# Kernel optimization log

Measured on AMD Instinct MI355X. Metric: run time of the kernel, lower is better.

The kernel has to match this reference:

```python
import jax, jax.numpy as jnp
import numpy as np

TAU = 2.0
V_TH = 1.0
ATAN_ALPHA = 2.0
LN_EPS = 1e-5

# Surrogate-gradient spike: forward = Heaviside(v - v_th), backward = ATan surrogate
@jax.custom_vjp
def atan_spike(x):
    return (x >= 0.0).astype(x.dtype)

def _atan_spike_fwd(x):
    return atan_spike(x), x

def _atan_spike_bwd(x, g):
    grad = ATAN_ALPHA / (2.0 * (1.0 + (jnp.pi / 2.0 * ATAN_ALPHA * x) ** 2))
    return (g * grad,)

atan_spike.defvjp(_atan_spike_fwd, _atan_spike_bwd)

def layernorm(x, g, b):
    m = jnp.mean(x, axis=-1, keepdims=True)
    v = jnp.mean((x - m) ** 2, axis=-1, keepdims=True)
    return (x - m) * jax.lax.rsqrt(v + LN_EPS) * g + b

def lif_multistep(x_btd):
    """spikingjelly LIFNode: decay_input=True, v_reset=0.0 (hard reset), detach_reset=True.
    x_btd: [B, T, D]; scan over T with membrane state [B, D]; returns spikes [B, T, D]."""
    x_tbd = jnp.swapaxes(x_btd, 0, 1)  # [T, B, D]
    def step(v, xt):
        h = v + (xt - v) / TAU                      # charge (decay_input, v_reset=0)
        s = atan_spike(h - V_TH)                    # fire
        v_new = h * (1.0 - jax.lax.stop_gradient(s))  # hard reset to 0, detached spike
        return v_new, s
    _, spikes = jax.lax.scan(step, jnp.zeros_like(x_tbd[0]), x_tbd)
    return jnp.swapaxes(spikes, 0, 1)  # [B, T, D]

def setup_inputs() -> dict:
    key = jax.random.key(0)
    ks = jax.random.split(key, 3)
    B, T, D, H = 256, 256, 128, 256
    x = jax.random.normal(ks[0], (B, T, D), dtype=jnp.float32)
    W1 = jax.random.normal(ks[1], (H, D), dtype=jnp.float32) * (1.0 / np.sqrt(D))
    b1 = jnp.zeros((H,), jnp.float32)
    g1 = jnp.ones((H,), jnp.float32)
    be1 = jnp.zeros((H,), jnp.float32)
    W2 = jax.random.normal(ks[2], (D, H), dtype=jnp.float32) * (1.0 / np.sqrt(H))
    b2 = jnp.zeros((D,), jnp.float32)
    g2 = jnp.ones((D,), jnp.float32)
    be2 = jnp.zeros((D,), jnp.float32)
    return {"x": x, "W1": W1, "b1": b1, "g1": g1, "be1": be1,
            "W2": W2, "b2": b2, "g2": g2, "be2": be2}

def reference(x, W1, b1, g1, be1, W2, b2, g2, be2):
    residual = x
    h = jnp.einsum("btd,hd->bth", x, W1) + b1
    h = layernorm(h, g1, be1)
    h = lif_multistep(h)            # dropout is identity at eval
    o = jnp.einsum("bth,dh->btd", h, W2) + b2
    o = layernorm(o, g2, be2)
    o = lif_multistep(o)
    return residual + o
```

## Files before the change

kernel.cpp:

```cpp
#include <hip/hip_runtime.h>
#include <hip/hip_bf16.h>
#include <stdint.h>

#define B_ 256
#define T_ 256
#define D_ 128
#define H_ 256
#define LN_EPS 1e-5

__global__ __launch_bounds__(256, 2) void k1_gemm_ln(
    const float* __restrict__ x, const float* __restrict__ W1,
    const float* __restrict__ b1, const float* __restrict__ g1, const float* __restrict__ be1,
    double* __restrict__ h1, int row0)
{
  __shared__ double As[16][64];
  __shared__ double Bs[16][256];
  const int tid = threadIdx.x;
  const int tx = tid & 31, ty = tid >> 5;
  const int orow = blockIdx.x * 64;
  const int grow = row0 + orow;

  double acc[8][8];
  #pragma unroll
  for (int i = 0; i < 8; ++i)
    #pragma unroll
    for (int j = 0; j < 8; ++j) acc[i][j] = 0.0;

  for (int kt = 0; kt < 128; kt += 16) {
    __syncthreads();
    {
      const int row = tid >> 2, ko = (tid & 3) * 4;
      const float4 f = *(const float4*)(x + (size_t)(grow + row) * 128 + kt + ko);
      As[ko+0][row] = (double)f.x; As[ko+1][row] = (double)f.y;
      As[ko+2][row] = (double)f.z; As[ko+3][row] = (double)f.w;
    }
    {
      const float* src = W1 + (size_t)tid * 128 + kt;
      #pragma unroll
      for (int j = 0; j < 4; ++j) {
        const float4 f = *(const float4*)(src + j*4);
        Bs[j*4+0][tid] = (double)f.x; Bs[j*4+1][tid] = (double)f.y;
        Bs[j*4+2][tid] = (double)f.z; Bs[j*4+3][tid] = (double)f.w;
      }
    }
    __syncthreads();
    #pragma unroll 2
    for (int k = 0; k < 16; ++k) {
      double a[8], b[8];
      #pragma unroll
      for (int j = 0; j < 4; ++j) {
        const double2 t2 = *(const double2*)&As[k][ty*8 + j*2];
        a[j*2] = t2.x; a[j*2+1] = t2.y;
      }
      #pragma unroll
      for (int c = 0; c < 4; ++c) {
        const double2 t2 = *(const double2*)&Bs[k][c*64 + tx*2];
        b[c*2] = t2.x; b[c*2+1] = t2.y;
      }
      #pragma unroll
      for (int i = 0; i < 8; ++i)
        #pragma unroll
        for (int j = 0; j < 8; ++j)
          acc[i][j] = fma(a[i], b[j], acc[i][j]);
    }
  }

  double gg[8], ee[8];
  #pragma unroll
  for (int j = 0; j < 8; ++j) {
    const int col = (j >> 1)*64 + tx*2 + (j & 1);
    const double bb = (double)b1[col];
    gg[j] = (double)g1[col]; ee[j] = (double)be1[col];
    #pragma unroll
    for (int i = 0; i < 8; ++i) acc[i][j] += bb;
  }
  #pragma unroll
  for (int i = 0; i < 8; ++i) {
    double s = 0.0, q = 0.0;
    #pragma unroll
    for (int j = 0; j < 8; ++j) { s += acc[i][j]; q += acc[i][j]*acc[i][j]; }
    #pragma unroll
    for (int m = 16; m >= 1; m >>= 1) { s += __shfl_xor(s, m, 64); q += __shfl_xor(q, m, 64); }
    const double mean = s * (1.0/256.0);
    const double var  = q * (1.0/256.0) - mean*mean;
    const double rstd = 1.0 / sqrt(var + LN_EPS);
    const int r = orow + ty*8 + i;
    #pragma unroll
    for (int c = 0; c < 4; ++c) {
      double2 o;
      o.x = (acc[i][c*2+0] - mean) * rstd * gg[c*2+0] + ee[c*2+0];
      o.y = (acc[i][c*2+1] - mean) * rstd * gg[c*2+1] + ee[c*2+1];
      *(double2*)&h1[(size_t)r*256 + c*64 + tx*2] = o;
    }
  }
}

__global__ __launch_bounds__(256) void k2_lif(
    const double* __restrict__ h1, uint8_t* __restrict__ s1)
{
  const int ci = blockIdx.x * 256 + threadIdx.x;
  const int b = ci >> 8, h = ci & 255;
  const double* p = h1 + (size_t)b * (T_*H_) + h;
  uint8_t* qp = s1 + (size_t)b * (T_*H_) + h;
  double v = 0.0;
  #pragma unroll 8
  for (int t = 0; t < T_; ++t) {
    const double xv = p[(size_t)t * H_];
    const double hm = v + (xv - v) * 0.5;
    const bool s = (hm >= 1.0);
    v = s ? 0.0 : hm;
    qp[(size_t)t * H_] = s ? (uint8_t)1 : (uint8_t)0;
  }
}

__global__ __launch_bounds__(256, 2) void k3_gemm_ln(
    const uint8_t* __restrict__ s1, const float* __restrict__ W2,
    const float* __restrict__ b2, const float* __restrict__ g2, const float* __restrict__ be2,
    double* __restrict__ h2)
{
  __shared__ double As[32][64];
  __shared__ double Bs[32][128];
  const int tid = threadIdx.x;
  const int tx = tid & 31, ty = tid >> 5;
  const int orow = blockIdx.x * 64;

  double acc[8][4];
  #pragma unroll
  for (int i = 0; i < 8; ++i)
    #pragma unroll
    for (int j = 0; j < 4; ++j) acc[i][j] = 0.0;

  for (int kt = 0; kt < 256; kt += 32) {
    __syncthreads();
    {
      const int row = tid >> 2, ko = (tid & 3) * 8;
      const uint2 u = *(const uint2*)(s1 + (size_t)(orow + row) * 256 + kt + ko);
      #pragma unroll
      for (int j = 0; j < 4; ++j) As[ko+j][row]   = (double)((u.x >> (8*j)) & 0xffu);
      #pragma unroll
      for (int j = 0; j < 4; ++j) As[ko+4+j][row] = (double)((u.y >> (8*j)) & 0xffu);
    }
    {
      const int col = tid >> 1, k0 = (tid & 1) * 16;
      const float* src = W2 + (size_t)col * 256 + kt + k0;
      #pragma unroll
      for (int j = 0; j < 4; ++j) {
        const float4 f = *(const float4*)(src + j*4);
        Bs[k0+j*4+0][col] = (double)f.x; Bs[k0+j*4+1][col] = (double)f.y;
        Bs[k0+j*4+2][col] = (double)f.z; Bs[k0+j*4+3][col] = (double)f.w;
      }
    }
    __syncthreads();
    #pragma unroll 2
    for (int k = 0; k < 32; ++k) {
      double a[8], b[4];
      #pragma unroll
      for (int j = 0; j < 4; ++j) {
        const double2 t2 = *(const double2*)&As[k][ty*8 + j*2];
        a[j*2] = t2.x; a[j*2+1] = t2.y;
      }
      #pragma unroll
      for (int c = 0; c < 2; ++c) {
        const double2 t2 = *(const double2*)&Bs[k][c*64 + tx*2];
        b[c*2] = t2.x; b[c*2+1] = t2.y;
      }
      #pragma unroll
      for (int i = 0; i < 8; ++i)
        #pragma unroll
        for (int j = 0; j < 4; ++j)
          acc[i][j] = fma(a[i], b[j], acc[i][j]);
    }
  }

  double gg[4], ee[4];
  #pragma unroll
  for (int j = 0; j < 4; ++j) {
    const int col = (j >> 1)*64 + tx*2 + (j & 1);
    const double bb = (double)b2[col];
    gg[j] = (double)g2[col]; ee[j] = (double)be2[col];
    #pragma unroll
    for (int i = 0; i < 8; ++i) acc[i][j] += bb;
  }
  #pragma unroll
  for (int i = 0; i < 8; ++i) {
    double s = 0.0, q = 0.0;
    #pragma unroll
    for (int j = 0; j < 4; ++j) { s += acc[i][j]; q += acc[i][j]*acc[i][j]; }
    #pragma unroll
    for (int m = 16; m >= 1; m >>= 1) { s += __shfl_xor(s, m, 64); q += __shfl_xor(q, m, 64); }
    const double mean = s * (1.0/128.0);
    const double var  = q * (1.0/128.0) - mean*mean;
    const double rstd = 1.0 / sqrt(var + LN_EPS);
    const int r = orow + ty*8 + i;
    #pragma unroll
    for (int c = 0; c < 2; ++c) {
      double2 o;
      o.x = (acc[i][c*2+0] - mean)*rstd*gg[c*2+0] + ee[c*2+0];
      o.y = (acc[i][c*2+1] - mean)*rstd*gg[c*2+1] + ee[c*2+1];
      *(double2*)&h2[(size_t)r*128 + c*64 + tx*2] = o;
    }
  }
}

__global__ __launch_bounds__(64) void k4_lif_res(
    const double* __restrict__ h2, const float* __restrict__ x,
    float* __restrict__ out, int row0)
{
  const int ci = blockIdx.x * 64 + threadIdx.x;
  const int b = ci >> 7, d = ci & 127;
  const double* p = h2 + (size_t)b * (T_*D_) + d;
  const size_t gbase = ((size_t)row0 + (size_t)b * T_) * D_ + d;
  double v = 0.0;
  #pragma unroll 8
  for (int t = 0; t < T_; ++t) {
    const double hv = p[(size_t)t * D_];
    const double hm = v + (hv - v) * 0.5;
    const bool s = (hm >= 1.0);
    v = s ? 0.0 : hm;
    out[gbase + (size_t)t * D_] = x[gbase + (size_t)t * D_] + (s ? 1.0f : 0.0f);
  }
}

extern "C" void kernel_launch(void* const* d_in, const int* in_sizes, int n_in,
                              void* d_out, int out_size, void* d_ws, size_t ws_size,
                              hipStream_t stream)
{
  const float* x   = (const float*)d_in[0];
  const float* W1  = (const float*)d_in[1];
  const float* b1  = (const float*)d_in[2];
  const float* g1  = (const float*)d_in[3];
  const float* be1 = (const float*)d_in[4];
  const float* W2  = (const float*)d_in[5];
  const float* b2  = (const float*)d_in[6];
  const float* g2  = (const float*)d_in[7];
  const float* be2 = (const float*)d_in[8];
  float* out = (float*)d_out;

  const size_t per_b = (size_t)T_*H_*sizeof(double) + (size_t)T_*H_ + (size_t)T_*D_*sizeof(double);
  int Bc = B_;
  while (Bc > 1 && (size_t)Bc * per_b > ws_size) Bc >>= 1;

  double*  h1 = (double*)d_ws;
  uint8_t* s1 = (uint8_t*)d_ws + (size_t)Bc*T_*H_*sizeof(double);
  double*  h2 = (double*)((uint8_t*)d_ws + (size_t)Bc*T_*H_*sizeof(double) + (size_t)Bc*T_*H_);

  const int nchunk = B_ / Bc;
  for (int c = 0; c < nchunk; ++c) {
    const int row0 = c * Bc * T_;
    k1_gemm_ln<<<dim3(Bc*4), dim3(256), 0, stream>>>(x, W1, b1, g1, be1, h1, row0);
    k2_lif   <<<dim3(Bc),   dim3(256), 0, stream>>>(h1, s1);
    k3_gemm_ln<<<dim3(Bc*4), dim3(256), 0, stream>>>(s1, W2, b2, g2, be2, h2);
    k4_lif_res<<<dim3(Bc*2), dim3(64),  0, stream>>>(h2, x, out, row0);
  }
}
```

Baseline: 333.3 us.

## Use FP64 MFMA 16x16x4 for both GEMM+LayerNorm kernels with runtime layout probe

Replaces the scalar FP64 FMA register-tiled GEMMs in k1 and k3 with __builtin_amdgcn_mfma_f64_16x16x4f64 matrix instructions, one 16-row strip per wave. A runtime probe discovers the accumulator row mapping and falls back to a scalar path if the layout is unexpected. Shared tiles are padded to reduce bank conflicts, and the k3 K-tile shrinks to 16. It aims to cut the dominant FP64 GEMM compute cost, at the price of probe overhead, scalar strided output stores, and heavier register use.

```diff
diff --git a/kernel.cpp b/kernel.cpp
--- a/kernel.cpp
+++ b/kernel.cpp
@@ -8,89 +8,153 @@
 #define H_ 256
 #define LN_EPS 1e-5
 
+typedef double f64x4 __attribute__((ext_vector_type(4)));
+
+__device__ __forceinline__ bool probe_f64_mfma_layout(int l16, int lg, int* rowp)
+{
+  const f64x4 zz = {0.0, 0.0, 0.0, 0.0};
+  const double pa_r = (lg == 0) ? (double)l16 : 0.0;
+  const double pb_1 = (lg == 0) ? 1.0 : 0.0;
+  const f64x4 prow = __builtin_amdgcn_mfma_f64_16x16x4f64(pa_r, pb_1, zz, 0, 0, 0);
+  const double pa_1 = (lg == 0) ? 1.0 : 0.0;
+  const double pb_c = (lg == 0) ? (double)l16 : 0.0;
+  const f64x4 pcol = __builtin_amdgcn_mfma_f64_16x16x4f64(pa_1, pb_c, zz, 0, 0, 0);
+  bool ok = true;
+  int rm = 0, rp = 0;
+  #pragma unroll
+  for (int r = 0; r < 4; ++r) {
+    const int ri = (int)prow[r];
+    const int ci = (int)pcol[r];
+    rowp[r] = ri;
+    ok = ok && ((double)ri == prow[r]) && (ri >= 0) && (ri < 16);
+    ok = ok && ((double)ci == pcol[r]) && (ci == l16);
+    rm |= 1 << ri;
+    rp |= ri << (4 * r);
+  }
+  ok = ok && (__popc(rm) == 4);
+  #pragma unroll
+  for (int m = 1; m <= 8; m <<= 1)
+    ok = ok && (__shfl_xor(rp, m, 64) == rp);
+  int rmw = rm;
+  rmw |= __shfl_xor(rmw, 16, 64);
+  rmw |= __shfl_xor(rmw, 32, 64);
+  ok = ok && (rmw == 0xFFFF);
+  return __all((int)ok) != 0;
+}
+
 __global__ __launch_bounds__(256, 2) void k1_gemm_ln(
     const float* __restrict__ x, const float* __restrict__ W1,
     const float* __restrict__ b1, const float* __restrict__ g1, const float* __restrict__ be1,
     double* __restrict__ h1, int row0)
 {
-  __shared__ double As[16][64];
-  __shared__ double Bs[16][256];
-  const int tid = threadIdx.x;
-  const int tx = tid & 31, ty = tid >> 5;
+  __shared__ double As[16 * 66];
+  __shared__ double Bs[16 * 258];
+  const int tid  = threadIdx.x;
+  const int lane = tid & 63, wave = tid >> 6;
+  const int l16  = lane & 15, lg = lane >> 4;
   const int orow = blockIdx.x * 64;
   const int grow = row0 + orow;
-
-  double acc[8][8];
-  #pragma unroll
-  for (int i = 0; i < 8; ++i)
-    #pragma unroll
-    for (int j = 0; j < 8; ++j) acc[i][j] = 0.0;
-
-  for (int kt = 0; kt < 128; kt += 16) {
+  const int wrow = wave * 16;
+
+  int rowp[4];
+  const bool ok = probe_f64_mfma_layout(l16, lg, rowp);
+
+  auto stage = [&](int kt) {
     __syncthreads();
     {
       const int row = tid >> 2, ko = (tid & 3) * 4;
       const float4 f = *(const float4*)(x + (size_t)(grow + row) * 128 + kt + ko);
-      As[ko+0][row] = (double)f.x; As[ko+1][row] = (double)f.y;
-      As[ko+2][row] = (double)f.z; As[ko+3][row] = (double)f.w;
+      As[(ko+0)*66 + row] = (double)f.x;
+      As[(ko+1)*66 + row] = (double)f.y;
+      As[(ko+2)*66 + row] = (double)f.z;
+      As[(ko+3)*66 + row] = (double)f.w;
     }
     {
       const float* src = W1 + (size_t)tid * 128 + kt;
       #pragma unroll
       for (int j = 0; j < 4; ++j) {
-        const float4 f = *(const float4*)(src + j*4);
-        Bs[j*4+0][tid] = (double)f.x; Bs[j*4+1][tid] = (double)f.y;
-        Bs[j*4+2][tid] = (double)f.z; Bs[j*4+3][tid] = (double)f.w;
+        const float4 f = *(const float4*)(src + j * 4);
+        Bs[(j*4+0)*258 + tid] = (double)f.x;
+        Bs[(j*4+1)*258 + tid] = (double)f.y;
+        Bs[(j*4+2)*258 + tid] = (double)f.z;
+        Bs[(j*4+3)*258 + tid] = (double)f.w;
       }
     }
     __syncthreads();
-    #pragma unroll 2
-    for (int k = 0; k < 16; ++k) {
-      double a[8], b[8];
-      #pragma unroll
-      for (int j = 0; j < 4; ++j) {
-        const double2 t2 = *(const double2*)&As[k][ty*8 + j*2];
-        a[j*2] = t2.x; a[j*2+1] = t2.y;
-      }
-      #pragma unroll
-      for (int c = 0; c < 4; ++c) {
-        const double2 t2 = *(const double2*)&Bs[k][c*64 + tx*2];
-        b[c*2] = t2.x; b[c*2+1] = t2.y;
-      }
-      #pragma unroll
-      for (int i = 0; i < 8; ++i)
+  };
+
+  if (ok) {
+    f64x4 acc[16];
+    #pragma unroll
+    for (int ct = 0; ct < 16; ++ct) acc[ct] = (f64x4){0.0, 0.0, 0.0, 0.0};
+    for (int kt = 0; kt < 128; kt += 16) {
+      stage(kt);
+      #pragma unroll
+      for (int ks = 0; ks < 4; ++ks) {
+        const int k = ks * 4 + lg;
+        const double a = As[k*66 + wrow + l16];
         #pragma unroll
-        for (int j = 0; j < 8; ++j)
-          acc[i][j] = fma(a[i], b[j], acc[i][j]);
-    }
-  }
-
-  double gg[8], ee[8];
-  #pragma unroll
-  for (int j = 0; j < 8; ++j) {
-    const int col = (j >> 1)*64 + tx*2 + (j & 1);
-    const double bb = (double)b1[col];
-    gg[j] = (double)g1[col]; ee[j] = (double)be1[col];
-    #pragma unroll
-    for (int i = 0; i < 8; ++i) acc[i][j] += bb;
-  }
-  #pragma unroll
-  for (int i = 0; i < 8; ++i) {
+        for (int ct = 0; ct < 16; ++ct) {
+          const double b = Bs[k*258 + ct*16 + l16];
+          acc[ct] = __builtin_amdgcn_mfma_f64_16x16x4f64(a, b, acc[ct], 0, 0, 0);
+        }
+      }
+    }
+    double bb[16];
+    #pragma unroll
+    for (int ct = 0; ct < 16; ++ct) bb[ct] = (double)b1[ct*16 + l16];
+    #pragma unroll
+    for (int r = 0; r < 4; ++r) {
+      double s = 0.0, q = 0.0;
+      #pragma unroll
+      for (int ct = 0; ct < 16; ++ct) {
+        const double v = acc[ct][r] + bb[ct];
+        s += v; q += v * v;
+      }
+      s += __shfl_xor(s, 1, 64); q += __shfl_xor(q, 1, 64);
+      s += __shfl_xor(s, 2, 64); q += __shfl_xor(q, 2, 64);
+      s += __shfl_xor(s, 4, 64); q += __shfl_xor(q, 4, 64);
+      s += __shfl_xor(s, 8, 64); q += __shfl_xor(q, 8, 64);
+      const double mean = s * (1.0/256.0);
+      const double var  = q * (1.0/256.0) - mean*mean;
+      const double rstd = 1.0 / sqrt(var + LN_EPS);
+      const int row = orow + wrow + rowp[r];
+      #pragma unroll
+      for (int ct = 0; ct < 16; ++ct) {
+        const int col = ct*16 + l16;
+        const double v = acc[ct][r] + bb[ct];
+        h1[(size_t)row*256 + col] = (v - mean) * rstd * (double)g1[col] + (double)be1[col];
+      }
+    }
+  } else {
+    double accv[64];
+    #pragma unroll
+    for (int c = 0; c < 64; ++c) accv[c] = 0.0;
+    for (int kt = 0; kt < 128; kt += 16) {
+      stage(kt);
+      for (int k = 0; k < 16; ++k) {
+        const double a = As[k*66 + wrow + l16];
+        #pragma unroll
+        for (int c = 0; c < 64; ++c)
+          accv[c] = fma(a, Bs[k*258 + lg*64 + c], accv[c]);
+      }
+    }
     double s = 0.0, q = 0.0;
     #pragma unroll
-    for (int j = 0; j < 8; ++j) { s += acc[i][j]; q += acc[i][j]*acc[i][j]; }
-    #pragma unroll
-    for (int m = 16; m >= 1; m >>= 1) { s += __shfl_xor(s, m, 64); q += __shfl_xor(q, m, 64); }
+    for (int c = 0; c < 64; ++c) {
+      accv[c] += (double)b1[lg*64 + c];
+      s += accv[c]; q += accv[c]*accv[c];
+    }
+    s += __shfl_xor(s, 16, 64); q += __shfl_xor(q, 16, 64);
+    s += __shfl_xor(s, 32, 64); q += __shfl_xor(q, 32, 64);
     const double mean = s * (1.0/256.0);
     const double var  = q * (1.0/256.0) - mean*mean;
     const double rstd = 1.0 / sqrt(var + LN_EPS);
-    const int r = orow + ty*8 + i;
-    #pragma unroll
-    for (int c = 0; c < 4; ++c) {
-      double2 o;
-      o.x = (acc[i][c*2+0] - mean) * rstd * gg[c*2+0] + ee[c*2+0];
-      o.y = (acc[i][c*2+1] - mean) * rstd * gg[c*2+1] + ee[c*2+1];
-      *(double2*)&h1[(size_t)r*256 + c*64 + tx*2] = o;
+    const int row = orow + wrow + l16;
+    #pragma unroll
+    for (int c = 0; c < 64; ++c) {
+      const int col = lg*64 + c;
+      h1[(size_t)row*256 + col] = (accv[c] - mean) * rstd * (double)g1[col] + (double)be1[col];
     }
   }
 }
@@ -118,86 +182,114 @@
     const float* __restrict__ b2, const float* __restrict__ g2, const float* __restrict__ be2,
     double* __restrict__ h2)
 {
-  __shared__ double As[32][64];
-  __shared__ double Bs[32][128];
-  const int tid = threadIdx.x;
-  const int tx = tid & 31, ty = tid >> 5;
+  __shared__ double As[16 * 66];
+  __shared__ double Bs[16 * 130];
+  const int tid  = threadIdx.x;
+  const int lane = tid & 63, wave = tid >> 6;
+  const int l16  = lane & 15, lg = lane >> 4;
   const int orow = blockIdx.x * 64;
-
-  double acc[8][4];
-  #pragma unroll
-  for (int i = 0; i < 8; ++i)
-    #pragma unroll
-    for (int j = 0; j < 4; ++j) acc[i][j] = 0.0;
-
-  for (int kt = 0; kt < 256; kt += 32) {
+  const int wrow = wave * 16;
+
+  int rowp[4];
+  const bool ok = probe_f64_mfma_layout(l16, lg, rowp);
+
+  auto stage = [&](int kt) {
     __syncthreads();
     {
-      const int row = tid >> 2, ko = (tid & 3) * 8;
-      const uint2 u = *(const uint2*)(s1 + (size_t)(orow + row) * 256 + kt + ko);
-      #pragma unroll
-      for (int j = 0; j < 4; ++j) As[ko+j][row]   = (double)((u.x >> (8*j)) & 0xffu);
-      #pragma unroll
-      for (int j = 0; j < 4; ++j) As[ko+4+j][row] = (double)((u.y >> (8*j)) & 0xffu);
+      const int row = tid >> 2, ko = (tid & 3) * 4;
+      const uint32_t u = *(const uint32_t*)(s1 + (size_t)(orow + row) * 256 + kt + ko);
+      As[(ko+0)*66 + row] = (double)( u        & 0xffu);
+      As[(ko+1)*66 + row] = (double)((u >> 8)  & 0xffu);
+      As[(ko+2)*66 + row] = (double)((u >> 16) & 0xffu);
+      As[(ko+3)*66 + row] = (double)((u >> 24) & 0xffu);
     }
     {
-      const int col = tid >> 1, k0 = (tid & 1) * 16;
+      const int col = tid >> 1, k0 = (tid & 1) * 8;
       const float* src = W2 + (size_t)col * 256 + kt + k0;
       #pragma unroll
-      for (int j = 0; j < 4; ++j) {
-        const float4 f = *(const float4*)(src + j*4);
-        Bs[k0+j*4+0][col] = (double)f.x; Bs[k0+j*4+1][col] = (double)f.y;
-        Bs[k0+j*4+2][col] = (double)f.z; Bs[k0+j*4+3][col] = (double)f.w;
+      for (int j = 0; j < 2; ++j) {
+        const float4 f = *(const float4*)(src + j * 4);
+        Bs[(k0+j*4+0)*130 + col] = (double)f.x;
+        Bs[(k0+j*4+1)*130 + col] = (double)f.y;
+        Bs[(k0+j*4+2)*130 + col] = (double)f.z;
+        Bs[(k0+j*4+3)*130 + col] = (double)f.w;
       }
     }
     __syncthreads();
-    #pragma unroll 2
-    for (int k = 0; k < 32; ++k) {
-      double a[8], b[4];
-      #pragma unroll
-      for (int j = 0; j < 4; ++j) {
-        const double2 t2 = *(const double2*)&As[k][ty*8 + j*2];
-        a[j*2] = t2.x; a[j*2+1] = t2.y;
-      }
-      #pragma unroll
-      for (int c = 0; c < 2; ++c) {
-        const double2 t2 = *(const double2*)&Bs[k][c*64 + tx*2];
-        b[c*2] = t2.x; b[c*2+1] = t2.y;
-      }
-      #pragma unroll
-      for (int i = 0; i < 8; ++i)
+  };
+
+  if (ok) {
+    f64x4 acc[8];
+    #pragma unroll
+    for (int ct = 0; ct < 8; ++ct) acc[ct] = (f64x4){0.0, 0.0, 0.0, 0.0};
+    for (int kt = 0; kt < 256; kt += 16) {
+      stage(kt);
+      #pragma unroll
+      for (int ks = 0; ks < 4; ++ks) {
+        const int k = ks * 4 + lg;
+        const double a = As[k*66 + wrow + l16];
         #pragma unroll
-        for (int j = 0; j < 4; ++j)
-          acc[i][j] = fma(a[i], b[j], acc[i][j]);
-    }
-  }
-
-  double gg[4], ee[4];
-  #pragma unroll
-  for (int j = 0; j < 4; ++j) {
-    const int col = (j >> 1)*64 + tx*2 + (j & 1);
-    const double bb = (double)b2[col];
-    gg[j] = (double)g2[col]; ee[j] = (double)be2[col];
-    #pragma unroll
-    for (int i = 0; i < 8; ++i) acc[i][j] += bb;
-  }
-  #pragma unroll
-  for (int i = 0; i < 8; ++i) {
+        for (int ct = 0; ct < 8; ++ct) {
+          const double b = Bs[k*130 + ct*16 + l16];
+          acc[ct] = __builtin_amdgcn_mfma_f64_16x16x4f64(a, b, acc[ct], 0, 0, 0);
+        }
+      }
+    }
+    double bb[8];
+    #pragma unroll
+    for (int ct = 0; ct < 8; ++ct) bb[ct] = (double)b2[ct*16 + l16];
+    #pragma unroll
+    for (int r = 0; r < 4; ++r) {
+      double s = 0.0, q = 0.0;
+      #pragma unroll
+      for (int ct = 0; ct < 8; ++ct) {
+        const double v = acc[ct][r] + bb[ct];
+        s += v; q += v * v;
+      }
+      s += __shfl_xor(s, 1, 64); q += __shfl_xor(q, 1, 64);
+      s += __shfl_xor(s, 2, 64); q += __shfl_xor(q, 2, 64);
+      s += __shfl_xor(s, 4, 64); q += __shfl_xor(q, 4, 64);
+      s += __shfl_xor(s, 8, 64); q += __shfl_xor(q, 8, 64);
+      const double mean = s * (1.0/128.0);
+      const double var  = q * (1.0/128.0) - mean*mean;
+      const double rstd = 1.0 / sqrt(var + LN_EPS);
+      const int row = orow + wrow + rowp[r];
+      #pragma unroll
+      for (int ct = 0; ct < 8; ++ct) {
+        const int col = ct*16 + l16;
+        const double v = acc[ct][r] + bb[ct];
+        h2[(size_t)row*128 + col] = (v - mean) * rstd * (double)g2[col] + (double)be2[col];
+      }
+    }
+  } else {
+    double accv[32];
+    #pragma unroll
+    for (int c = 0; c < 32; ++c) accv[c] = 0.0;
+    for (int kt = 0; kt < 256; kt += 16) {
+      stage(kt);
+      for (int k = 0; k < 16; ++k) {
+        const double a = As[k*66 + wrow + l16];
+        #pragma unroll
+        for (int c = 0; c < 32; ++c)
+          accv[c] = fma(a, Bs[k*130 + lg*32 + c], accv[c]);
+      }
+    }
     double s = 0.0, q = 0.0;
     #pragma unroll
-    for (int j = 0; j < 4; ++j) { s += acc[i][j]; q += acc[i][j]*acc[i][j]; }
-    #pragma unroll
-    for (int m = 16; m >= 1; m >>= 1) { s += __shfl_xor(s, m, 64); q += __shfl_xor(q, m, 64); }
+    for (int c = 0; c < 32; ++c) {
+      accv[c] += (double)b2[lg*32 + c];
+      s += accv[c]; q += accv[c]*accv[c];
+    }
+    s += __shfl_xor(s, 16, 64); q += __shfl_xor(q, 16, 64);
+    s += __shfl_xor(s, 32, 64); q += __shfl_xor(q, 32, 64);
     const double mean = s * (1.0/128.0);
     const double var  = q * (1.0/128.0) - mean*mean;
     const double rstd = 1.0 / sqrt(var + LN_EPS);
-    const int r = orow + ty*8 + i;
-    #pragma unroll
-    for (int c = 0; c < 2; ++c) {
-      double2 o;
-      o.x = (acc[i][c*2+0] - mean)*rstd*gg[c*2+0] + ee[c*2+0];
-      o.y = (acc[i][c*2+1] - mean)*rstd*gg[c*2+1] + ee[c*2+1];
-      *(double2*)&h2[(size_t)r*128 + c*64 + tx*2] = o;
+    const int row = orow + wrow + l16;
+    #pragma unroll
+    for (int c = 0; c < 32; ++c) {
+      const int col = lg*32 + c;
+      h2[(size_t)row*128 + col] = (accv[c] - mean) * rstd * (double)g2[col] + (double)be2[col];
     }
   }
 }
```

New measurement: 309.9 us. 7.0% less time.
